# Optimization experiments

Measured on AMD Instinct MI355X. Metric: run time of the kernel, lower is better.

## Reference

```python
import jax, jax.numpy as jnp
import numpy as np

TEMPERATURE = 16.0  # sqrt(d_k) for d_k=256

def setup_inputs() -> dict:
    key = jax.random.key(0)
    q = jax.random.normal(key, (32, 1024, 256), dtype=jnp.float32)
    return {"q": q}

def reference(q):
    # attn = q @ q^T  (b, l, l)
    attn = jnp.einsum('bld,bmd->blm', q, q)
    # data-dependent zero mask -> -inf fill (before temperature scaling, matching torch order)
    zero_mask = attn == 0.0
    attn = jnp.where(zero_mask, -jnp.inf, attn / TEMPERATURE)
    attn = jax.nn.softmax(attn, axis=2)
    # rows that were fully -inf produce NaN -> zero them out
    attn = jnp.where(jnp.isnan(attn), 0.0, attn)
    # dropout is identity in eval/reference mode
    output = jnp.einsum('blm,bmd->bld', attn, q)
    return (output, attn)
```

## Files before the change

kernel.cpp:

```cpp
#include <hip/hip_runtime.h>
#include <stdint.h>

#define NB 32
#define NL 1024
#define ND 256
#define ROWU16 2048

typedef __attribute__((ext_vector_type(8))) __bf16 bf16x8;
typedef __attribute__((ext_vector_type(4))) float f32x4;

__device__ __forceinline__ uint16_t f2bf(float f) {
  union { float f; uint32_t u; } v; v.f = f;
  return (uint16_t)((v.u + 0x7fffu + ((v.u >> 16) & 1u)) >> 16);
}
__device__ __forceinline__ float bf2f(uint16_t h) {
  union { uint32_t u; float f; } v; v.u = ((uint32_t)h) << 16;
  return v.f;
}

#define GLD_LDS16(g, l)                                                        \
  __builtin_amdgcn_global_load_lds(                                            \
      (__attribute__((address_space(1))) void*)(g),                            \
      (__attribute__((address_space(3))) void*)(l), 16, 0, 0)

__global__ __launch_bounds__(256) void convert_kernel(
    const float* __restrict__ q, uint16_t* __restrict__ qb,
    uint16_t* __restrict__ qt) {
  __shared__ uint16_t tile[64][72];
  int b = blockIdx.z;
  int l0 = blockIdx.x * 64, d0 = blockIdx.y * 64;
  int t = threadIdx.x;
  int r = t >> 4;
  int c4 = (t & 15) * 4;
  const float* qsrc = q + (size_t)b * NL * ND;
  uint16_t* qbb = qb + (size_t)b * NL * ND;
  uint16_t* qtb = qt + (size_t)b * ND * NL;
#pragma unroll
  for (int i = 0; i < 4; i++) {
    int row = r + 16 * i;
    float4 v = *(const float4*)(qsrc + (size_t)(l0 + row) * ND + d0 + c4);
    ushort4 h;
    h.x = f2bf(v.x); h.y = f2bf(v.y); h.z = f2bf(v.z); h.w = f2bf(v.w);
    *(ushort4*)(qbb + (size_t)(l0 + row) * ND + d0 + c4) = h;
    tile[row][c4 + 0] = h.x; tile[row][c4 + 1] = h.y;
    tile[row][c4 + 2] = h.z; tile[row][c4 + 3] = h.w;
  }
  __syncthreads();
#pragma unroll
  for (int i = 0; i < 4; i++) {
    int drow = r + 16 * i;
    ushort4 h;
    h.x = tile[c4 + 0][drow]; h.y = tile[c4 + 1][drow];
    h.z = tile[c4 + 2][drow]; h.w = tile[c4 + 3][drow];
    *(ushort4*)(qtb + (size_t)(d0 + drow) * NL + l0 + c4) = h;
  }
}

__global__ __launch_bounds__(256) void qk_kernel(
    const uint16_t* __restrict__ qb, float* __restrict__ attn_f32) {
  __shared__ alignas(16) uint16_t As[128 * 32];
  __shared__ alignas(16) uint16_t Bs[128 * 32];
  __shared__ float rp[128][2];
  int b = blockIdx.z;
  int m0 = blockIdx.x * 128, n0 = blockIdx.y * 128;
  const uint16_t* Q = qb + (size_t)b * NL * ND;
  int tid = threadIdx.x, lane = tid & 63, wave = tid >> 6;
  int wm = (wave & 1) * 64, wn = (wave >> 1) * 64;
  int quad = lane >> 4, l15 = lane & 15;
  f32x4 acc[4][4] = {};

  for (int k0 = 0; k0 < ND; k0 += 32) {
    __syncthreads();
#pragma unroll
    for (int i = 0; i < 2; i++) {
      int c = i * 256 + wave * 64 + lane;
      int row = c >> 2, cc = c & 3;
      int sw = (row >> 1) & 3;
      int gc = k0 + ((cc ^ sw) * 8);
      GLD_LDS16(Q + (size_t)(m0 + row) * ND + gc,
                As + (size_t)(i * 256 + wave * 64) * 8);
      GLD_LDS16(Q + (size_t)(n0 + row) * ND + gc,
                Bs + (size_t)(i * 256 + wave * 64) * 8);
    }
    __syncthreads();
    bf16x8 af[4], bfr[4];
#pragma unroll
    for (int t = 0; t < 4; t++) {
      int ra = wm + t * 16 + l15;
      af[t] = *(const bf16x8*)(As + ra * 32 + ((quad ^ ((ra >> 1) & 3)) * 8));
      int rb = wn + t * 16 + l15;
      bfr[t] = *(const bf16x8*)(Bs + rb * 32 + ((quad ^ ((rb >> 1) & 3)) * 8));
    }
#pragma unroll
    for (int tm = 0; tm < 4; tm++)
#pragma unroll
      for (int tn = 0; tn < 4; tn++)
        acc[tm][tn] = __builtin_amdgcn_mfma_f32_16x16x32_bf16(
            af[tm], bfr[tn], acc[tm][tn], 0, 0, 0);
  }

  const float kf = 0.09016844005555f;
  uint16_t* attn_u16 = (uint16_t*)attn_f32;
  size_t gbase = (size_t)b * NL;
#pragma unroll
  for (int tm = 0; tm < 4; tm++) {
    int rbl = wm + tm * 16 + quad * 4;
    float rsum[4] = {0.f, 0.f, 0.f, 0.f};
#pragma unroll
    for (int tn = 0; tn < 4; tn++) {
      int col = n0 + wn + tn * 16 + l15;
#pragma unroll
      for (int j = 0; j < 4; j++) {
        float s = acc[tm][tn][j];
        float e = (s == 0.0f) ? 0.0f : __builtin_amdgcn_exp2f(s * kf);
        attn_u16[(gbase + m0 + rbl + j) * ROWU16 + col] = f2bf(e);
        rsum[j] += e;
      }
    }
#pragma unroll
    for (int j = 0; j < 4; j++) {
      float v = rsum[j];
      v += __shfl_xor(v, 1, 64);
      v += __shfl_xor(v, 2, 64);
      v += __shfl_xor(v, 4, 64);
      v += __shfl_xor(v, 8, 64);
      if (l15 == 0) rp[rbl + j][wave >> 1] = v;
    }
  }
  __syncthreads();
  if (tid < 128) {
    float s = rp[tid][0] + rp[tid][1];
    attn_f32[(gbase + m0 + tid) * (size_t)NL + 512 + blockIdx.y] = s;
  }
}

__global__ __launch_bounds__(256) void pv_kernel(
    const float* __restrict__ attn_f32, const uint16_t* __restrict__ qt,
    float* __restrict__ out) {
  __shared__ alignas(16) uint16_t As[128 * 32];
  __shared__ alignas(16) uint16_t Bs[128 * 32];
  __shared__ float inv_lds[128];
  int b = blockIdx.z;
  int m0 = blockIdx.x * 128, d0 = blockIdx.y * 128;
  const uint16_t* Ap = (const uint16_t*)attn_f32 + (size_t)b * NL * ROWU16;
  const uint16_t* Bt = qt + (size_t)b * ND * NL;
  int tid = threadIdx.x, lane = tid & 63, wave = tid >> 6;
  int wm = (wave & 1) * 64, wn = (wave >> 1) * 64;
  int quad = lane >> 4, l15 = lane & 15;
  f32x4 acc[4][4] = {};

  if (tid < 128) {
    const float* pf =
        attn_f32 + (size_t)(b * NL + m0 + tid) * NL + 512;
    float s = pf[0] + pf[1] + pf[2] + pf[3] + pf[4] + pf[5] + pf[6] + pf[7];
    inv_lds[tid] = (s > 0.0f) ? 1.0f / s : 0.0f;
  }

  for (int k0 = 0; k0 < NL; k0 += 32) {
    __syncthreads();
#pragma unroll
    for (int i = 0; i < 2; i++) {
      int c = i * 256 + wave * 64 + lane;
      int row = c >> 2, cc = c & 3;
      int sw = (row >> 1) & 3;
      int gc = k0 + ((cc ^ sw) * 8);
      GLD_LDS16(Ap + (size_t)(m0 + row) * ROWU16 + gc,
                As + (size_t)(i * 256 + wave * 64) * 8);
      GLD_LDS16(Bt + (size_t)(d0 + row) * NL + gc,
                Bs + (size_t)(i * 256 + wave * 64) * 8);
    }
    __syncthreads();
    bf16x8 af[4], bfr[4];
#pragma unroll
    for (int t = 0; t < 4; t++) {
      int ra = wm + t * 16 + l15;
      af[t] = *(const bf16x8*)(As + ra * 32 + ((quad ^ ((ra >> 1) & 3)) * 8));
      int rb = wn + t * 16 + l15;
      bfr[t] = *(const bf16x8*)(Bs + rb * 32 + ((quad ^ ((rb >> 1) & 3)) * 8));
    }
#pragma unroll
    for (int tm = 0; tm < 4; tm++)
#pragma unroll
      for (int tn = 0; tn < 4; tn++)
        acc[tm][tn] = __builtin_amdgcn_mfma_f32_16x16x32_bf16(
            af[tm], bfr[tn], acc[tm][tn], 0, 0, 0);
  }

  float* O = out + (size_t)b * NL * ND;
#pragma unroll
  for (int tm = 0; tm < 4; tm++) {
    int rbl = wm + tm * 16 + quad * 4;
#pragma unroll
    for (int tn = 0; tn < 4; tn++) {
      int col = d0 + wn + tn * 16 + l15;
#pragma unroll
      for (int j = 0; j < 4; j++)
        O[(size_t)(m0 + rbl + j) * ND + col] = acc[tm][tn][j] * inv_lds[rbl + j];
    }
  }
}

__global__ __launch_bounds__(256) void scale_kernel(float* __restrict__ attn_f32) {
  size_t g = blockIdx.x;
  const uint16_t* u = (const uint16_t*)attn_f32 + g * ROWU16;
  float* f = attn_f32 + g * (size_t)NL;
  int t = threadIdx.x;
  ushort4 h = ((const ushort4*)u)[t];
  float s = f[512] + f[513] + f[514] + f[515] +
            f[516] + f[517] + f[518] + f[519];
  float inv = (s > 0.0f) ? 1.0f / s : 0.0f;
  __syncthreads();
  float4 v;
  v.x = bf2f(h.x) * inv; v.y = bf2f(h.y) * inv;
  v.z = bf2f(h.z) * inv; v.w = bf2f(h.w) * inv;
  ((float4*)f)[t] = v;
}

extern "C" void kernel_launch(void* const* d_in, const int* in_sizes, int n_in,
                              void* d_out, int out_size, void* d_ws,
                              size_t ws_size, hipStream_t stream) {
  (void)in_sizes; (void)n_in; (void)out_size; (void)ws_size;
  const float* q = (const float*)d_in[0];
  float* out = (float*)d_out;
  float* attn = out + (size_t)NB * NL * ND;
  uint16_t* qb = (uint16_t*)d_ws;
  uint16_t* qt = qb + (size_t)NB * NL * ND;

  convert_kernel<<<dim3(16, 4, NB), 256, 0, stream>>>(q, qb, qt);
  qk_kernel<<<dim3(8, 8, NB), 256, 0, stream>>>(qb, attn);
  pv_kernel<<<dim3(8, 2, NB), 256, 0, stream>>>(attn, qt, out);
  scale_kernel<<<NB * NL, 256, 0, stream>>>(attn);
}
```

Measured before the change: 271.1 us.

## Stage full-K B tile in LDS and hold A in registers for QK; widen PV K-step

qk_kernel now loads the A operand for the full 256-deep K dimension straight from global memory into registers. It stages the entire 128x256 B tile in LDS with a single load phase and one barrier, which removes the per-K-step sync loop. pv_kernel doubles its K tile from 32 to 64 with an XOR swizzle, halving the number of barrier-separated load iterations. The costs are heavy register use for the A fragments (32 bf16x8 per thread) and 64KB of LDS per QK block, which may reduce occupancy, plus the loss of load/compute overlap in QK.

```diff
diff --git a/kernel.cpp b/kernel.cpp
--- a/kernel.cpp
+++ b/kernel.cpp
@@ -58,8 +58,7 @@
 
 __global__ __launch_bounds__(256) void qk_kernel(
     const uint16_t* __restrict__ qb, float* __restrict__ attn_f32) {
-  __shared__ alignas(16) uint16_t As[128 * 32];
-  __shared__ alignas(16) uint16_t Bs[128 * 32];
+  __shared__ alignas(16) uint16_t Bs[128 * 256];
   __shared__ float rp[128][2];
   int b = blockIdx.z;
   int m0 = blockIdx.x * 128, n0 = blockIdx.y * 128;
@@ -67,36 +66,41 @@
   int tid = threadIdx.x, lane = tid & 63, wave = tid >> 6;
   int wm = (wave & 1) * 64, wn = (wave >> 1) * 64;
   int quad = lane >> 4, l15 = lane & 15;
+
+  bf16x8 af[4][8];
+#pragma unroll
+  for (int tm = 0; tm < 4; tm++) {
+    const uint16_t* ap = Q + (size_t)(m0 + wm + tm * 16 + l15) * ND + quad * 8;
+#pragma unroll
+    for (int kg = 0; kg < 8; kg++) af[tm][kg] = *(const bf16x8*)(ap + kg * 32);
+  }
+
+#pragma unroll
+  for (int i = 0; i < 16; i++) {
+    int ch = i * 256 + wave * 64 + lane;
+    int r = ch >> 5, cl = ch & 31;
+    int cg = cl ^ (r & 7);
+    GLD_LDS16(Q + (size_t)(n0 + r) * ND + cg * 8,
+              Bs + (size_t)(i * 256 + wave * 64) * 8);
+  }
+  __syncthreads();
+
   f32x4 acc[4][4] = {};
-
-  for (int k0 = 0; k0 < ND; k0 += 32) {
-    __syncthreads();
-#pragma unroll
-    for (int i = 0; i < 2; i++) {
-      int c = i * 256 + wave * 64 + lane;
-      int row = c >> 2, cc = c & 3;
-      int sw = (row >> 1) & 3;
-      int gc = k0 + ((cc ^ sw) * 8);
-      GLD_LDS16(Q + (size_t)(m0 + row) * ND + gc,
-                As + (size_t)(i * 256 + wave * 64) * 8);
-      GLD_LDS16(Q + (size_t)(n0 + row) * ND + gc,
-                Bs + (size_t)(i * 256 + wave * 64) * 8);
-    }
-    __syncthreads();
-    bf16x8 af[4], bfr[4];
-#pragma unroll
-    for (int t = 0; t < 4; t++) {
-      int ra = wm + t * 16 + l15;
-      af[t] = *(const bf16x8*)(As + ra * 32 + ((quad ^ ((ra >> 1) & 3)) * 8));
-      int rb = wn + t * 16 + l15;
-      bfr[t] = *(const bf16x8*)(Bs + rb * 32 + ((quad ^ ((rb >> 1) & 3)) * 8));
+#pragma unroll
+  for (int kg = 0; kg < 8; kg++) {
+    bf16x8 bfr[4];
+#pragma unroll
+    for (int tn = 0; tn < 4; tn++) {
+      int rb = wn + tn * 16 + l15;
+      int c = (kg * 4 + quad) ^ (rb & 7);
+      bfr[tn] = *(const bf16x8*)(Bs + rb * 256 + c * 8);
     }
 #pragma unroll
     for (int tm = 0; tm < 4; tm++)
 #pragma unroll
       for (int tn = 0; tn < 4; tn++)
         acc[tm][tn] = __builtin_amdgcn_mfma_f32_16x16x32_bf16(
-            af[tm], bfr[tn], acc[tm][tn], 0, 0, 0);
+            af[tm][kg], bfr[tn], acc[tm][tn], 0, 0, 0);
   }
 
   const float kf = 0.09016844005555f;
@@ -137,8 +141,8 @@
 __global__ __launch_bounds__(256) void pv_kernel(
     const float* __restrict__ attn_f32, const uint16_t* __restrict__ qt,
     float* __restrict__ out) {
-  __shared__ alignas(16) uint16_t As[128 * 32];
-  __shared__ alignas(16) uint16_t Bs[128 * 32];
+  __shared__ alignas(16) uint16_t As[128 * 64];
+  __shared__ alignas(16) uint16_t Bs[128 * 64];
   __shared__ float inv_lds[128];
   int b = blockIdx.z;
   int m0 = blockIdx.x * 128, d0 = blockIdx.y * 128;
@@ -150,40 +154,41 @@
   f32x4 acc[4][4] = {};
 
   if (tid < 128) {
-    const float* pf =
-        attn_f32 + (size_t)(b * NL + m0 + tid) * NL + 512;
+    const float* pf = attn_f32 + (size_t)(b * NL + m0 + tid) * NL + 512;
     float s = pf[0] + pf[1] + pf[2] + pf[3] + pf[4] + pf[5] + pf[6] + pf[7];
     inv_lds[tid] = (s > 0.0f) ? 1.0f / s : 0.0f;
   }
 
-  for (int k0 = 0; k0 < NL; k0 += 32) {
+  for (int k0 = 0; k0 < NL; k0 += 64) {
     __syncthreads();
 #pragma unroll
-    for (int i = 0; i < 2; i++) {
-      int c = i * 256 + wave * 64 + lane;
-      int row = c >> 2, cc = c & 3;
-      int sw = (row >> 1) & 3;
-      int gc = k0 + ((cc ^ sw) * 8);
-      GLD_LDS16(Ap + (size_t)(m0 + row) * ROWU16 + gc,
+    for (int i = 0; i < 4; i++) {
+      int ch = i * 256 + wave * 64 + lane;
+      int r = ch >> 3, cl = ch & 7;
+      int cg = cl ^ (r & 7);
+      GLD_LDS16(Ap + (size_t)(m0 + r) * ROWU16 + k0 + cg * 8,
                 As + (size_t)(i * 256 + wave * 64) * 8);
-      GLD_LDS16(Bt + (size_t)(d0 + row) * NL + gc,
+      GLD_LDS16(Bt + (size_t)(d0 + r) * NL + k0 + cg * 8,
                 Bs + (size_t)(i * 256 + wave * 64) * 8);
     }
     __syncthreads();
-    bf16x8 af[4], bfr[4];
-#pragma unroll
-    for (int t = 0; t < 4; t++) {
-      int ra = wm + t * 16 + l15;
-      af[t] = *(const bf16x8*)(As + ra * 32 + ((quad ^ ((ra >> 1) & 3)) * 8));
-      int rb = wn + t * 16 + l15;
-      bfr[t] = *(const bf16x8*)(Bs + rb * 32 + ((quad ^ ((rb >> 1) & 3)) * 8));
-    }
-#pragma unroll
-    for (int tm = 0; tm < 4; tm++)
-#pragma unroll
-      for (int tn = 0; tn < 4; tn++)
-        acc[tm][tn] = __builtin_amdgcn_mfma_f32_16x16x32_bf16(
-            af[tm], bfr[tn], acc[tm][tn], 0, 0, 0);
+#pragma unroll
+    for (int kg = 0; kg < 2; kg++) {
+      bf16x8 af[4], bfr[4];
+#pragma unroll
+      for (int t = 0; t < 4; t++) {
+        int ra = wm + t * 16 + l15;
+        af[t] = *(const bf16x8*)(As + ra * 64 + (((kg * 4 + quad) ^ (ra & 7)) * 8));
+        int rb = wn + t * 16 + l15;
+        bfr[t] = *(const bf16x8*)(Bs + rb * 64 + (((kg * 4 + quad) ^ (rb & 7)) * 8));
+      }
+#pragma unroll
+      for (int tm = 0; tm < 4; tm++)
+#pragma unroll
+        for (int tn = 0; tn < 4; tn++)
+          acc[tm][tn] = __builtin_amdgcn_mfma_f32_16x16x32_bf16(
+              af[tm], bfr[tn], acc[tm][tn], 0, 0, 0);
+    }
   }
 
   float* O = out + (size_t)b * NL * ND;
```

Measured after the change: 285.0 us. +5.1%, slower.
